# Optimization experiments

Measured on AMD Instinct MI355X. Metric: run time of the kernel, lower is better.

Reference implementation:

```python
import jax, jax.numpy as jnp
import numpy as np

N_UU_LAYERS = 2
N_II_LAYERS = 2
ALPHA = 0.5
BETA = 0.5


def _sym_norm(edge_index, n):
    # PyG gcn_norm without self loops: norm = deg^-1/2[row] * deg^-1/2[col]
    row, col = edge_index[0], edge_index[1]
    deg = jax.ops.segment_sum(jnp.ones(row.shape, jnp.float32), col, num_segments=n)
    dinv = jnp.where(deg > 0, jax.lax.rsqrt(jnp.maximum(deg, 1e-12)), 0.0)
    return dinv[row] * dinv[col]


def _propagate(x, edge_index, norm, n):
    # gather from source, weight by norm, scatter-sum into target
    row, col = edge_index[0], edge_index[1]
    return jax.ops.segment_sum(norm[:, None] * x[row], col, num_segments=n)


def setup_inputs() -> dict:
    key = jax.random.key(0)
    ks = jax.random.split(key, 16)
    U, I, D, R, S = 50000, 50000, 64, 5, 2
    E_REL, E_SIM, B = 1000000, 1600000, 8192
    sc = 0.1  # xavier-ish scale for d=64
    return {
        "Gu": jax.random.normal(ks[0], (U, D), jnp.float32) * sc,
        "Gi": jax.random.normal(ks[1], (I, D), jnp.float32) * sc,
        "Gus": jax.random.normal(ks[2], (U, D), jnp.float32) * sc,
        "Gis": jax.random.normal(ks[3], (I, D), jnp.float32) * sc,
        "W_conv": jax.random.normal(ks[4], (R, D, D), jnp.float32) * sc,
        "W_dense": jax.random.normal(ks[5], (D, D), jnp.float32) * sc,
        "P": jax.random.normal(ks[6], (S, D, D), jnp.float32) * sc,
        "A": jax.random.uniform(ks[7], (R, S), jnp.float32),
        "relations": jnp.arange(1, R + 1, dtype=jnp.float32),
        "edge_index_rel": jax.random.randint(ks[8], (R, 2, E_REL), 0, U + I, jnp.int32),
        "edge_index_uu": jax.random.randint(ks[9], (2, E_SIM), 0, U, jnp.int32),
        "edge_index_ii": jax.random.randint(ks[10], (2, E_SIM), 0, I, jnp.int32),
        "user": jax.random.randint(ks[11], (B,), 0, U, jnp.int32),
        "item": jax.random.randint(ks[12], (B,), 0, I, jnp.int32),
    }


def reference(Gu, Gi, Gus, Gis, W_conv, W_dense, P, A, relations,
              edge_index_rel, edge_index_uu, edge_index_ii, user, item):
    U, I = Gu.shape[0], Gi.shape[0]
    N = U + I
    R = W_conv.shape[0]

    # LGConv stacks on user-user and item-item similarity graphs
    norm_uu = _sym_norm(edge_index_uu, U)
    gus = Gus
    for _ in range(N_UU_LAYERS):
        gus = _propagate(gus, edge_index_uu, norm_uu, U)
    norm_ii = _sym_norm(edge_index_ii, I)
    gis = Gis
    for _ in range(N_II_LAYERS):
        gis = _propagate(gis, edge_index_ii, norm_ii, I)

    # Per-relation GCNConv (1 layer, linear-then-aggregate, ReLU), sum accumulation
    x0 = jnp.concatenate([Gu, Gi], axis=0)  # [N, D]
    acc = jnp.zeros((N, W_conv.shape[2]), x0.dtype)
    for r in range(R):
        ei = edge_index_rel[r]
        norm = _sym_norm(ei, N)
        xr = x0 @ W_conv[r]
        xr = jax.nn.relu(_propagate(xr, ei, norm, N))
        acc = acc + xr

    emb = acc @ W_dense  # dense layer, no bias; dropout p=0
    zu, zi = emb[:U], emb[U:]

    # batch gather and blend with similarity-propagated embeddings
    gu = (1.0 - ALPHA) * zu[user] + ALPHA * gus[user]
    gi_b = (1.0 - BETA) * zi[item] + BETA * gis[item]

    # basis-weighted bilinear scoring per relation
    Q = jnp.einsum('rs,sde->rde', A, P)             # [R, D, D]
    pui = jnp.einsum('bd,rde,be->br', gu, Q, gi_b)  # [B, R]
    xui = jnp.sum(relations * jax.nn.softmax(pui, axis=1), axis=1)
    return (xui, pui)
```

## Files before the change

### kernel.cpp

```cpp
#include <hip/hip_runtime.h>
#include <hip/hip_bf16.h>

#define DD 64
#define C_REL 40
#define C_SIM 80

static inline int cdiv(long long a, long long b) { return (int)((a + b - 1) / b); }

__global__ void k_scatter_pad(const int* __restrict__ row, const int* __restrict__ col, int E,
                              int* __restrict__ cnt, int* __restrict__ edp, int C) {
    int e = blockIdx.x * blockDim.x + threadIdx.x;
    if (e >= E) return;
    int r = row[e], c = col[e];
    int pos = atomicAdd(&cnt[c], 1);
    if (pos < C) edp[(size_t)c * C + pos] = r;
}

__global__ void k_dinv_i(const int* __restrict__ cnt, float* __restrict__ dinv, int n) {
    int i = blockIdx.x * blockDim.x + threadIdx.x;
    if (i < n) { int d = cnt[i]; dinv[i] = d > 0 ? rsqrtf((float)d) : 0.f; }
}

__global__ __launch_bounds__(256) void k_gather_pad(const float* __restrict__ src, float* __restrict__ dst,
                                                    const int* __restrict__ edp, const int* __restrict__ cnt,
                                                    const float* __restrict__ dinv, int C, int nNodes) {
    int t = blockIdx.x * blockDim.x + threadIdx.x;
    int node = t >> 4;
    if (node >= nNodes) return;
    int k4 = (t & 15) << 2;
    int deg = cnt[node]; if (deg > C) deg = C;
    float dc = dinv[node];
    const int* lst = edp + (size_t)node * C;
    float4 acc = make_float4(0.f, 0.f, 0.f, 0.f);
    for (int e = 0; e < deg; ++e) {
        int rs = lst[e];
        float nn = dc * dinv[rs];
        float4 v = *(const float4*)(src + (size_t)rs * DD + k4);
        acc.x += nn * v.x; acc.y += nn * v.y; acc.z += nn * v.z; acc.w += nn * v.w;
    }
    *(float4*)(dst + (size_t)node * DD + k4) = acc;
}

__global__ __launch_bounds__(256) void k_gather_sel_sim(const float* __restrict__ src, float* __restrict__ dst,
                                                        const int* __restrict__ edp, const int* __restrict__ cnt,
                                                        const float* __restrict__ dinv, int C,
                                                        const int* __restrict__ idx, int B) {
    int t = blockIdx.x * blockDim.x + threadIdx.x;
    int j = t >> 4;
    if (j >= B) return;
    int k4 = (t & 15) << 2;
    int node = idx[j];
    int deg = cnt[node]; if (deg > C) deg = C;
    float dc = dinv[node];
    const int* lst = edp + (size_t)node * C;
    float4 acc = make_float4(0.f, 0.f, 0.f, 0.f);
    for (int e = 0; e < deg; ++e) {
        int rs = lst[e];
        float nn = dc * dinv[rs];
        float4 v = *(const float4*)(src + (size_t)rs * DD + k4);
        acc.x += nn * v.x; acc.y += nn * v.y; acc.z += nn * v.z; acc.w += nn * v.w;
    }
    *(float4*)(dst + (size_t)j * DD + k4) = acc;
}

__global__ __launch_bounds__(256) void k_gather_sel_rel(const float* __restrict__ src, float* __restrict__ ACC,
                                                        const int* __restrict__ edp, const int* __restrict__ cnt,
                                                        const float* __restrict__ dinv, int C,
                                                        const int* __restrict__ user, const int* __restrict__ item,
                                                        int B, int U) {
    int t = blockIdx.x * blockDim.x + threadIdx.x;
    int j = t >> 4;
    if (j >= 2 * B) return;
    int k4 = (t & 15) << 2;
    int node = (j < B) ? user[j] : (U + item[j - B]);
    int deg = cnt[node]; if (deg > C) deg = C;
    float dc = dinv[node];
    const int* lst = edp + (size_t)node * C;
    float4 acc = make_float4(0.f, 0.f, 0.f, 0.f);
    for (int e = 0; e < deg; ++e) {
        int rs = lst[e];
        float nn = dc * dinv[rs];
        float4 v = *(const float4*)(src + (size_t)rs * DD + k4);
        acc.x += nn * v.x; acc.y += nn * v.y; acc.z += nn * v.z; acc.w += nn * v.w;
    }
    float4* o = (float4*)(ACC + (size_t)j * DD + k4);
    float4 cur = *o;
    cur.x += fmaxf(acc.x, 0.f); cur.y += fmaxf(acc.y, 0.f);
    cur.z += fmaxf(acc.z, 0.f); cur.w += fmaxf(acc.w, 0.f);
    *o = cur;
}


__global__ __launch_bounds__(256) void k_matmul64(const float* __restrict__ X0, const float* __restrict__ X1,
                                                  int split, const float* __restrict__ W,
                                                  float* __restrict__ out, int Nrows) {
    __shared__ float Wl[64 * 64];
    int tid = threadIdx.x;
    for (int t = tid; t < 1024; t += 256) ((float4*)Wl)[t] = ((const float4*)W)[t];
    __syncthreads();
    int row = blockIdx.x * 64 + (tid >> 2);
    if (row >= Nrows) return;
    const float* xs = (row < split) ? (X0 + (size_t)row * DD) : (X1 + (size_t)(row - split) * DD);
    int j0 = (tid & 3) << 4;
    float acc[16];
#pragma unroll
    for (int j = 0; j < 16; ++j) acc[j] = 0.f;
#pragma unroll 4
    for (int k = 0; k < 64; k += 4) {
        float4 xv = *(const float4*)(xs + k);
        const float* w0 = Wl + k * 64 + j0;
#pragma unroll
        for (int j = 0; j < 16; ++j) acc[j] += xv.x * w0[j];
#pragma unroll
        for (int j = 0; j < 16; ++j) acc[j] += xv.y * w0[64 + j];
#pragma unroll
        for (int j = 0; j < 16; ++j) acc[j] += xv.z * w0[128 + j];
#pragma unroll
        for (int j = 0; j < 16; ++j) acc[j] += xv.w * w0[192 + j];
    }
    float* o = out + (size_t)row * DD + j0;
#pragma unroll
    for (int j = 0; j < 4; ++j)
        ((float4*)o)[j] = make_float4(acc[4 * j], acc[4 * j + 1], acc[4 * j + 2], acc[4 * j + 3]);
}

__global__ void k_blend(const float* __restrict__ gus_sel, const float* __restrict__ gis_sel,
                        const float* __restrict__ EMB, float* __restrict__ gu, float* __restrict__ gi,
                        int B) {
    int t = blockIdx.x * blockDim.x + threadIdx.x;
    if (t >= 2 * B * 16) return;
    int j = t >> 4, k = t & 15;
    float4 e = ((const float4*)(EMB + (size_t)j * DD))[k];
    if (j < B) {
        float4 s = ((const float4*)(gus_sel + (size_t)j * DD))[k];
        ((float4*)(gu + (size_t)j * DD))[k] =
            make_float4(0.5f * (s.x + e.x), 0.5f * (s.y + e.y), 0.5f * (s.z + e.z), 0.5f * (s.w + e.w));
    } else {
        int jj = j - B;
        float4 s = ((const float4*)(gis_sel + (size_t)jj * DD))[k];
        ((float4*)(gi + (size_t)jj * DD))[k] =
            make_float4(0.5f * (s.x + e.x), 0.5f * (s.y + e.y), 0.5f * (s.z + e.z), 0.5f * (s.w + e.w));
    }
}

__global__ void k_build_Q(const float* __restrict__ A, const float* __restrict__ P,
                          float* __restrict__ Q, int R, int S) {
    int t = blockIdx.x * blockDim.x + threadIdx.x;
    if (t >= R * 4096) return;
    int r = t / 4096, de = t % 4096;
    float acc = 0.f;
    for (int s = 0; s < S; ++s) acc += A[r * S + s] * P[(size_t)s * 4096 + de];
    Q[t] = acc;
}

__global__ __launch_bounds__(256) void k_pui2(const float* __restrict__ gu, const float* __restrict__ gi,
                                              const float* __restrict__ Q, float* __restrict__ pout,
                                              int B, int R) {
    int wid = (int)(((long long)blockIdx.x * blockDim.x + threadIdx.x) >> 6);
    int lane = threadIdx.x & 63;
    if (wid >= B * R) return;
    int b = wid / R, r = wid % R;
    const float* Qr = Q + (size_t)r * 4096;
    float gu_l = gu[(size_t)b * DD + lane];
    float gi_l = gi[(size_t)b * DD + lane];
    float acc = 0.f;
#pragma unroll 8
    for (int d = 0; d < 64; ++d) {
        float gud = __shfl(gu_l, d, 64);
        acc += gud * Qr[d * 64 + lane];
    }
    acc *= gi_l;
#pragma unroll
    for (int off = 32; off > 0; off >>= 1) acc += __shfl_down(acc, off, 64);
    if (lane == 0) pout[wid] = acc;
}

__global__ void k_softmax_out(const float* __restrict__ pui, const float* __restrict__ rel,
                              float* __restrict__ xui, int B, int R) {
    int b = blockIdx.x * blockDim.x + threadIdx.x;
    if (b >= B) return;
    float m = -1e30f;
    for (int r = 0; r < R; ++r) m = fmaxf(m, pui[(size_t)b * R + r]);
    float se = 0.f, sw = 0.f;
    for (int r = 0; r < R; ++r) {
        float e = expf(pui[(size_t)b * R + r] - m);
        se += e; sw += rel[r] * e;
    }
    xui[b] = sw / se;
}

extern "C" void kernel_launch(void* const* d_in, const int* in_sizes, int n_in,
                              void* d_out, int out_size, void* d_ws, size_t ws_size,
                              hipStream_t stream) {
    const float* Gu      = (const float*)d_in[0];
    const float* Gi      = (const float*)d_in[1];
    const float* Gus     = (const float*)d_in[2];
    const float* Gis     = (const float*)d_in[3];
    const float* W_conv  = (const float*)d_in[4];
    const float* W_dense = (const float*)d_in[5];
    const float* P       = (const float*)d_in[6];
    const float* A       = (const float*)d_in[7];
    const float* rel     = (const float*)d_in[8];
    const int*   ei_rel  = (const int*)d_in[9];
    const int*   ei_uu   = (const int*)d_in[10];
    const int*   ei_ii   = (const int*)d_in[11];
    const int*   user    = (const int*)d_in[12];
    const int*   item    = (const int*)d_in[13];

    const int U = in_sizes[0] / DD;
    const int I = in_sizes[1] / DD;
    const int N = U + I;
    const int R = in_sizes[8];
    const int S = in_sizes[6] / 4096;
    const int E_REL = in_sizes[9] / (2 * R);
    const int E_SIM = in_sizes[10] / 2;
    const int B = in_sizes[12];
    const size_t RN = (size_t)R * N;

    size_t edpElems = (size_t)U * C_SIM;
    if ((size_t)I * C_SIM > edpElems) edpElems = (size_t)I * C_SIM;
    if ((size_t)N * C_REL > edpElems) edpElems = (size_t)N * C_REL;
    edpElems = (edpElems + 3) & ~(size_t)3;

    char* p = (char*)d_ws;
    int*   edp     = (int*)p;   p += edpElems * 4;
    int*   cnt     = (int*)p;   p += RN * 4;
    float* dinv    = (float*)p; p += RN * 4;
    float* gus_sel = (float*)p; p += (size_t)B * DD * 4;
    float* gis_sel = (float*)p; p += (size_t)B * DD * 4;
    float* ACC     = (float*)p; p += (size_t)2 * B * DD * 4;
    float* EMB     = (float*)p; p += (size_t)2 * B * DD * 4;
    float* gu      = (float*)p; p += (size_t)B * DD * 4;
    float* gi      = (float*)p; p += (size_t)B * DD * 4;
    float* Q       = (float*)p; p += (size_t)R * 4096 * 4;
    float* BIG0    = (float*)p; p += (size_t)N * DD * 4;

    float* xui = (float*)d_out;
    float* pui = (float*)d_out + B;

    const int BT = 256;

    hipMemsetAsync(cnt, 0, (size_t)(U + I) * 4, stream);
    k_scatter_pad<<<cdiv(E_SIM, BT), BT, 0, stream>>>(ei_uu, ei_uu + E_SIM, E_SIM, cnt, edp, C_SIM);
    k_dinv_i<<<cdiv(U, BT), BT, 0, stream>>>(cnt, dinv, U);
    k_gather_pad<<<cdiv((long long)U * 16, BT), BT, 0, stream>>>(Gus, BIG0, edp, cnt, dinv, C_SIM, U);
    k_gather_sel_sim<<<cdiv((long long)B * 16, BT), BT, 0, stream>>>(BIG0, gus_sel, edp, cnt, dinv, C_SIM, user, B);
    k_scatter_pad<<<cdiv(E_SIM, BT), BT, 0, stream>>>(ei_ii, ei_ii + E_SIM, E_SIM, cnt + U, edp, C_SIM);
    k_dinv_i<<<cdiv(I, BT), BT, 0, stream>>>(cnt + U, dinv + U, I);
    k_gather_pad<<<cdiv((long long)I * 16, BT), BT, 0, stream>>>(Gis, BIG0, edp, cnt + U, dinv + U, C_SIM, I);
    k_gather_sel_sim<<<cdiv((long long)B * 16, BT), BT, 0, stream>>>(BIG0, gis_sel, edp, cnt + U, dinv + U, C_SIM, item, B);

    hipMemsetAsync(cnt, 0, RN * 4, stream);
    hipMemsetAsync(ACC, 0, (size_t)2 * B * DD * 4, stream);
    for (int r = 0; r < R; ++r) {
        const int* rrow = ei_rel + (size_t)r * 2 * E_REL;
        const int* rcol = rrow + E_REL;
        k_scatter_pad<<<cdiv(E_REL, BT), BT, 0, stream>>>(rrow, rcol, E_REL, cnt + (size_t)r * N, edp, C_REL);
        k_dinv_i<<<cdiv(N, BT), BT, 0, stream>>>(cnt + (size_t)r * N, dinv + (size_t)r * N, N);
        k_matmul64<<<cdiv(N, 64), BT, 0, stream>>>(Gu, Gi, U, W_conv + (size_t)r * 4096, BIG0, N);
        k_gather_sel_rel<<<cdiv((long long)2 * B * 16, BT), BT, 0, stream>>>(BIG0, ACC, edp,
                                                                             cnt + (size_t)r * N, dinv + (size_t)r * N,
                                                                             C_REL, user, item, B, U);
    }

    k_matmul64<<<cdiv(2 * B, 64), BT, 0, stream>>>(ACC, ACC, 2 * B, W_dense, EMB, 2 * B);
    k_blend<<<cdiv((long long)2 * B * 16, BT), BT, 0, stream>>>(gus_sel, gis_sel, EMB, gu, gi, B);

    k_build_Q<<<cdiv((long long)R * 4096, BT), BT, 0, stream>>>(A, P, Q, R, S);
    k_pui2<<<cdiv((long long)B * R * 64, BT), BT, 0, stream>>>(gu, gi, Q, pui, B, R);
    k_softmax_out<<<cdiv(B, BT), BT, 0, stream>>>(pui, rel, xui, B, R);
}
```

Baseline: 1.124 ms.

## Aggregate raw embeddings before per-relation transform and scatter only selected nodes

```diff
diff --git a/kernel.cpp b/kernel.cpp
--- a/kernel.cpp
+++ b/kernel.cpp
@@ -6,6 +6,7 @@
 #define C_SIM 80
 
 static inline int cdiv(long long a, long long b) { return (int)((a + b - 1) / b); }
+
 
 __global__ void k_scatter_pad(const int* __restrict__ row, const int* __restrict__ col, int E,
                               int* __restrict__ cnt, int* __restrict__ edp, int C) {
@@ -16,10 +17,29 @@
     if (pos < C) edp[(size_t)c * C + pos] = r;
 }
 
+__global__ void k_scatter_rel(const int* __restrict__ row, const int* __restrict__ col, int E,
+                              int* __restrict__ cnt, int* __restrict__ edp, int C,
+                              const unsigned char* __restrict__ sel) {
+    int e = blockIdx.x * blockDim.x + threadIdx.x;
+    if (e >= E) return;
+    int r = row[e], c = col[e];
+    int pos = atomicAdd(&cnt[c], 1);
+    if (sel[c] && pos < C) edp[(size_t)c * C + pos] = r;
+}
+
+__global__ void k_mark(unsigned char* __restrict__ sel, const int* __restrict__ user,
+                       const int* __restrict__ item, int B, int U) {
+    int t = blockIdx.x * blockDim.x + threadIdx.x;
+    if (t >= 2 * B) return;
+    int node = (t < B) ? user[t] : (U + item[t - B]);
+    sel[node] = 1;
+}
+
 __global__ void k_dinv_i(const int* __restrict__ cnt, float* __restrict__ dinv, int n) {
     int i = blockIdx.x * blockDim.x + threadIdx.x;
     if (i < n) { int d = cnt[i]; dinv[i] = d > 0 ? rsqrtf((float)d) : 0.f; }
 }
+
 
 __global__ __launch_bounds__(256) void k_gather_pad(const float* __restrict__ src, float* __restrict__ dst,
                                                     const int* __restrict__ edp, const int* __restrict__ cnt,
@@ -63,44 +83,43 @@
     *(float4*)(dst + (size_t)j * DD + k4) = acc;
 }
 
-__global__ __launch_bounds__(256) void k_gather_sel_rel(const float* __restrict__ src, float* __restrict__ ACC,
-                                                        const int* __restrict__ edp, const int* __restrict__ cnt,
-                                                        const float* __restrict__ dinv, int C,
-                                                        const int* __restrict__ user, const int* __restrict__ item,
-                                                        int B, int U) {
+__global__ __launch_bounds__(256) void k_gather_x0_rel(const float* __restrict__ Gu, const float* __restrict__ Gi,
+                                                       int U, float* __restrict__ TMP,
+                                                       const int* __restrict__ edp, const int* __restrict__ cnt,
+                                                       int C, const int* __restrict__ user,
+                                                       const int* __restrict__ item, int B) {
     int t = blockIdx.x * blockDim.x + threadIdx.x;
     int j = t >> 4;
     if (j >= 2 * B) return;
     int k4 = (t & 15) << 2;
     int node = (j < B) ? user[j] : (U + item[j - B]);
-    int deg = cnt[node]; if (deg > C) deg = C;
-    float dc = dinv[node];
+    int cn = cnt[node];
+    int deg = cn > C ? C : cn;
+    float dc = cn > 0 ? rsqrtf((float)cn) : 0.f;
     const int* lst = edp + (size_t)node * C;
     float4 acc = make_float4(0.f, 0.f, 0.f, 0.f);
     for (int e = 0; e < deg; ++e) {
         int rs = lst[e];
-        float nn = dc * dinv[rs];
-        float4 v = *(const float4*)(src + (size_t)rs * DD + k4);
+        int cr = cnt[rs];
+        float nn = dc * (cr > 0 ? rsqrtf((float)cr) : 0.f);
+        const float* srow = (rs < U) ? (Gu + (size_t)rs * DD) : (Gi + (size_t)(rs - U) * DD);
+        float4 v = *(const float4*)(srow + k4);
         acc.x += nn * v.x; acc.y += nn * v.y; acc.z += nn * v.z; acc.w += nn * v.w;
     }
-    float4* o = (float4*)(ACC + (size_t)j * DD + k4);
-    float4 cur = *o;
-    cur.x += fmaxf(acc.x, 0.f); cur.y += fmaxf(acc.y, 0.f);
-    cur.z += fmaxf(acc.z, 0.f); cur.w += fmaxf(acc.w, 0.f);
-    *o = cur;
-}
-
-
-__global__ __launch_bounds__(256) void k_matmul64(const float* __restrict__ X0, const float* __restrict__ X1,
-                                                  int split, const float* __restrict__ W,
-                                                  float* __restrict__ out, int Nrows) {
+    *(float4*)(TMP + (size_t)j * DD + k4) = acc;
+}
+
+
+template <bool RELU_ACC>
+__global__ __launch_bounds__(256) void k_matmul64t(const float* __restrict__ X, const float* __restrict__ W,
+                                                   float* __restrict__ out, int Nrows) {
     __shared__ float Wl[64 * 64];
     int tid = threadIdx.x;
     for (int t = tid; t < 1024; t += 256) ((float4*)Wl)[t] = ((const float4*)W)[t];
     __syncthreads();
     int row = blockIdx.x * 64 + (tid >> 2);
     if (row >= Nrows) return;
-    const float* xs = (row < split) ? (X0 + (size_t)row * DD) : (X1 + (size_t)(row - split) * DD);
+    const float* xs = X + (size_t)row * DD;
     int j0 = (tid & 3) << 4;
     float acc[16];
 #pragma unroll
@@ -119,9 +138,21 @@
         for (int j = 0; j < 16; ++j) acc[j] += xv.w * w0[192 + j];
     }
     float* o = out + (size_t)row * DD + j0;
-#pragma unroll
-    for (int j = 0; j < 4; ++j)
-        ((float4*)o)[j] = make_float4(acc[4 * j], acc[4 * j + 1], acc[4 * j + 2], acc[4 * j + 3]);
+    if (RELU_ACC) {
+#pragma unroll
+        for (int j = 0; j < 4; ++j) {
+            float4 cur = ((float4*)o)[j];
+            cur.x += fmaxf(acc[4 * j + 0], 0.f);
+            cur.y += fmaxf(acc[4 * j + 1], 0.f);
+            cur.z += fmaxf(acc[4 * j + 2], 0.f);
+            cur.w += fmaxf(acc[4 * j + 3], 0.f);
+            ((float4*)o)[j] = cur;
+        }
+    } else {
+#pragma unroll
+        for (int j = 0; j < 4; ++j)
+            ((float4*)o)[j] = make_float4(acc[4 * j], acc[4 * j + 1], acc[4 * j + 2], acc[4 * j + 3]);
+    }
 }
 
 __global__ void k_blend(const float* __restrict__ gus_sel, const float* __restrict__ gis_sel,
@@ -222,18 +253,22 @@
     if ((size_t)N * C_REL > edpElems) edpElems = (size_t)N * C_REL;
     edpElems = (edpElems + 3) & ~(size_t)3;
 
+    int maxUI = U > I ? U : I;
+
     char* p = (char*)d_ws;
     int*   edp     = (int*)p;   p += edpElems * 4;
     int*   cnt     = (int*)p;   p += RN * 4;
-    float* dinv    = (float*)p; p += RN * 4;
+    float* dinv    = (float*)p; p += (size_t)(U + I) * 4;
+    unsigned char* sel = (unsigned char*)p; p += ((size_t)N + 15) & ~(size_t)15;
     float* gus_sel = (float*)p; p += (size_t)B * DD * 4;
     float* gis_sel = (float*)p; p += (size_t)B * DD * 4;
     float* ACC     = (float*)p; p += (size_t)2 * B * DD * 4;
+    float* TMP     = (float*)p; p += (size_t)2 * B * DD * 4;
     float* EMB     = (float*)p; p += (size_t)2 * B * DD * 4;
     float* gu      = (float*)p; p += (size_t)B * DD * 4;
     float* gi      = (float*)p; p += (size_t)B * DD * 4;
     float* Q       = (float*)p; p += (size_t)R * 4096 * 4;
-    float* BIG0    = (float*)p; p += (size_t)N * DD * 4;
+    float* BIG0    = (float*)p; p += (size_t)maxUI * DD * 4;
 
     float* xui = (float*)d_out;
     float* pui = (float*)d_out + B;
@@ -251,19 +286,20 @@
     k_gather_sel_sim<<<cdiv((long long)B * 16, BT), BT, 0, stream>>>(BIG0, gis_sel, edp, cnt + U, dinv + U, C_SIM, item, B);
 
     hipMemsetAsync(cnt, 0, RN * 4, stream);
+    hipMemsetAsync(sel, 0, (size_t)N, stream);
     hipMemsetAsync(ACC, 0, (size_t)2 * B * DD * 4, stream);
+    k_mark<<<cdiv(2 * B, BT), BT, 0, stream>>>(sel, user, item, B, U);
     for (int r = 0; r < R; ++r) {
         const int* rrow = ei_rel + (size_t)r * 2 * E_REL;
         const int* rcol = rrow + E_REL;
-        k_scatter_pad<<<cdiv(E_REL, BT), BT, 0, stream>>>(rrow, rcol, E_REL, cnt + (size_t)r * N, edp, C_REL);
-        k_dinv_i<<<cdiv(N, BT), BT, 0, stream>>>(cnt + (size_t)r * N, dinv + (size_t)r * N, N);
-        k_matmul64<<<cdiv(N, 64), BT, 0, stream>>>(Gu, Gi, U, W_conv + (size_t)r * 4096, BIG0, N);
-        k_gather_sel_rel<<<cdiv((long long)2 * B * 16, BT), BT, 0, stream>>>(BIG0, ACC, edp,
-                                                                             cnt + (size_t)r * N, dinv + (size_t)r * N,
-                                                                             C_REL, user, item, B, U);
-    }
-
-    k_matmul64<<<cdiv(2 * B, 64), BT, 0, stream>>>(ACC, ACC, 2 * B, W_dense, EMB, 2 * B);
+        k_scatter_rel<<<cdiv(E_REL, BT), BT, 0, stream>>>(rrow, rcol, E_REL, cnt + (size_t)r * N, edp, C_REL, sel);
+        k_gather_x0_rel<<<cdiv((long long)2 * B * 16, BT), BT, 0, stream>>>(Gu, Gi, U, TMP, edp,
+                                                                            cnt + (size_t)r * N, C_REL,
+                                                                            user, item, B);
+        k_matmul64t<true><<<cdiv(2 * B, 64), BT, 0, stream>>>(TMP, W_conv + (size_t)r * 4096, ACC, 2 * B);
+    }
+
+    k_matmul64t<false><<<cdiv(2 * B, 64), BT, 0, stream>>>(ACC, W_dense, EMB, 2 * B);
     k_blend<<<cdiv((long long)2 * B * 16, BT), BT, 0, stream>>>(gus_sel, gis_sel, EMB, gu, gi, B);
 
     k_build_Q<<<cdiv((long long)R * 4096, BT), BT, 0, stream>>>(A, P, Q, R, S);
```

After: 958.1 us. 1.17x faster.
